# Optimization experiments

Measured on AMD Instinct MI355X. Metric: run time of the kernel, lower is better.

## Reference

```python
import jax, jax.numpy as jnp
import numpy as np

B, D = 8, 36          # batch, spatial extent of each of the 4 dims
KOUT = D - 2          # VALID conv with kernel 3 -> 34

_DN = jax.lax.ConvDimensionNumbers(lhs_spec=(0, 1, 2, 3, 4, 5),
                                   rhs_spec=(0, 1, 2, 3, 4, 5),
                                   out_spec=(0, 1, 2, 3, 4, 5))

def _conv4d(x, w):
    # x: [B, Cin, D,D,D,D], w: [Cout, Cin, 3,3,3,3] -> [B, Cout, D-2,...]
    return jax.lax.conv_general_dilated(x, w, window_strides=(1, 1, 1, 1),
                                        padding='VALID', dimension_numbers=_DN)

def setup_inputs() -> dict:
    key = jax.random.key(0)
    ks = jax.random.split(key, 8)
    fan_in = 1 * 3 ** 4  # 81 taps
    return {
        'x_real': jax.random.normal(ks[0], (B, 1, D, D, D, D), jnp.float32),
        'x_imag': jax.random.normal(ks[1], (B, 1, D, D, D, D), jnp.float32),
        'w_real': jax.random.normal(ks[2], (2, 1, 3, 3, 3, 3), jnp.float32) / np.sqrt(fan_in),
        'w_imag': jax.random.normal(ks[3], (2, 1, 3, 3, 3, 3), jnp.float32) / np.sqrt(fan_in),
        'b_real': jax.random.normal(ks[4], (2,), jnp.float32) * 0.1,
        'b_imag': jax.random.normal(ks[5], (2,), jnp.float32) * 0.1,
        'head_w': jax.random.normal(ks[6], (1, KOUT), jnp.float32) / np.sqrt(KOUT),
        'head_b': jax.random.normal(ks[7], (1,), jnp.float32) * 0.1,
    }

def reference(x_real, x_imag, w_real, w_imag, b_real, b_imag, head_w, head_b):
    bshape = (1, -1, 1, 1, 1, 1)
    # complex 4D conv: (Wr + iWi) * (xr + ixi)
    yr = _conv4d(x_real, w_real) - _conv4d(x_imag, w_imag) + b_real.reshape(bshape)
    yi = _conv4d(x_real, w_imag) + _conv4d(x_imag, w_real) + b_imag.reshape(bshape)
    # CReLU: ReLU on real and imaginary parts independently
    yr = jax.nn.relu(yr)
    yi = jax.nn.relu(yi)
    # Modulus (tiny eps keeps grad finite at 0, matching practical impls)
    m = jnp.sqrt(yr * yr + yi * yi + 1e-12)  # [B, 2, 34,34,34,34]
    # Linear(out=1) over the last spatial dim, then sigmoid
    h = jnp.einsum('bcdefw,ow->bcdefo', m, head_w) + head_b
    out = jax.nn.sigmoid(h)[:, 0]  # drop channel dim -> [B, 34, 34, 34, 1]
    return out
```

## Files before the change

kernel.cpp:

```cpp
#include <hip/hip_runtime.h>
#include <hip/hip_fp16.h>
#include <math.h>

namespace {
constexpr int DIN = 36, DOUT = 34;
constexpr int TE = 8, TF = 8;
constexpr int RE = 10, RF = 10;
constexpr int NROWS = 3*RE*RF;
constexpr int ROWW  = 38;
constexpr int NCHUNK = NROWS*9;
constexpr int BLOCKS_PER_B = 34*5*5;
constexpr int NBLOCKS = 8*BLOCKS_PER_B;
constexpr int NT = 512;
constexpr int SITER = (NCHUNK + NT - 1)/NT;
constexpr int D3 = DIN*DIN*DIN, D2 = DIN*DIN;
constexpr int WS_WPK  = 0;
constexpr int WS_SCAL = 216;
constexpr int WS_HW   = 220;
}

__device__ __forceinline__ unsigned div9u(unsigned n)   { return __umulhi(n, 0x38E38E39u) >> 1; }
__device__ __forceinline__ unsigned div100u(unsigned n) { return __umulhi(n, 0x51EB851Fu) >> 5; }
__device__ __forceinline__ unsigned div10u(unsigned n)  { return __umulhi(n, 0x66666667u) >> 2; }

__device__ __forceinline__ unsigned pack2h(float a, float b) {
    union { __half2 h; unsigned u; } x; x.h = __floats2half2_rn(a, b); return x.u;
}
__device__ __forceinline__ __half2 bch(unsigned u) {
    union { unsigned u; __half2 h; } x; x.u = u; return x.h;
}

__global__ void prep_kernel(const float* __restrict__ wr, const float* __restrict__ wi,
                            const float* __restrict__ br, const float* __restrict__ bi,
                            const float* __restrict__ hw, const float* __restrict__ hb,
                            unsigned* __restrict__ ws)
{
    const int t = threadIdx.x;
    if (t < 27) {
        uint4* p = reinterpret_cast<uint4*>(ws + WS_WPK);
        p[2*t]   = make_uint4(pack2h(wr[3*t],   -wi[3*t]),
                              pack2h(wr[3*t+1], -wi[3*t+1]),
                              pack2h(wr[3*t+2], -wi[3*t+2]), 0u);
        p[2*t+1] = make_uint4(pack2h(wi[3*t],    wr[3*t]),
                              pack2h(wi[3*t+1],  wr[3*t+1]),
                              pack2h(wi[3*t+2],  wr[3*t+2]), 0u);
    }
    if (t < DOUT) reinterpret_cast<float*>(ws)[WS_HW + t] = hw[t];
    if (t == 63) {
        float* s = reinterpret_cast<float*>(ws);
        s[WS_SCAL] = br[0]; s[WS_SCAL+1] = bi[0]; s[WS_SCAL+2] = hb[0];
    }
}

__device__ __forceinline__ void stage(const float* __restrict__ xr, const float* __restrict__ xi,
                                      unsigned* __restrict__ s_xu, int t, unsigned g0off)
{
    #pragma unroll
    for (int it = 0; it < SITER; ++it) {
        const int C = it*NT + t;
        if (C < NCHUNK) {
            const unsigned row = div9u((unsigned)C);
            const unsigned c   = (unsigned)C - row*9u;
            const unsigned rd  = div100u(row);
            const unsigned rem = row - rd*100u;
            const unsigned re  = div10u(rem);
            const unsigned rf  = rem - re*10u;
            const unsigned goff = g0off + rd*D3 + re*D2 + rf*DIN + c*4u;
            const float4 vr = *reinterpret_cast<const float4*>(xr + goff);
            const float4 vi = *reinterpret_cast<const float4*>(xi + goff);
            unsigned* dst = s_xu + row*ROWW + c*4;
            uint2 lo, hi;
            lo.x = pack2h(vr.x, vi.x); lo.y = pack2h(vr.y, vi.y);
            hi.x = pack2h(vr.z, vi.z); hi.y = pack2h(vr.w, vi.w);
            *reinterpret_cast<uint2*>(dst)     = lo;
            *reinterpret_cast<uint2*>(dst + 2) = hi;
        }
    }
}

template<int NW, int W0>
__device__ __forceinline__ float conv_group(const unsigned* __restrict__ s_xu,
                                            const uint4* __restrict__ wpk,
                                            const float* __restrict__ hws,
                                            int e, int f,
                                            float c_br, float c_bi, float hinit)
{
    constexpr int NL = (NW + 2 + 1)/2;
    __half2 accr[NW], acci[NW];
    #pragma unroll
    for (int w = 0; w < NW; ++w) {
        accr[w] = __floats2half2_rn(0.f, 0.f);
        acci[w] = __floats2half2_rn(0.f, 0.f);
    }

    const int abase = (e*RF + f)*ROWW + W0;

    #pragma unroll 1
    for (int i = 0; i < 3; ++i)
    #pragma unroll 1
    for (int j = 0; j < 3; ++j)
    {
        const unsigned* sp = s_xu + abase + (i*(RE*RF) + j*RF)*ROWW;
        const int tapb = (i*3 + j)*3;
        #pragma unroll
        for (int k = 0; k < 3; ++k)
        {
            uint2 q[NL];
            #pragma unroll
            for (int m = 0; m < NL; ++m)
                q[m] = *reinterpret_cast<const uint2*>(sp + k*ROWW + 2*m);
            const __half2* win = reinterpret_cast<const __half2*>(q);

            const uint4 wa = wpk[2*(tapb + k)];
            const uint4 wb = wpk[2*(tapb + k) + 1];
            #pragma unroll
            for (int l = 0; l < 3; ++l) {
                const __half2 WA = bch(l==0 ? wa.x : l==1 ? wa.y : wa.z);
                const __half2 WB = bch(l==0 ? wb.x : l==1 ? wb.y : wb.z);
                #pragma unroll
                for (int w = 0; w < NW; ++w) {
                    const __half2 x2 = win[w + l];
                    accr[w] = __hfma2(x2, WA, accr[w]);
                    acci[w] = __hfma2(x2, WB, acci[w]);
                }
            }
        }
    }

    float h = hinit;
    #pragma unroll
    for (int w = 0; w < NW; ++w) {
        const float yr = __low2float(accr[w]) + __high2float(accr[w]) + c_br;
        const float yi = __low2float(acci[w]) + __high2float(acci[w]) + c_bi;
        const float a = fmaxf(yr, 0.f);
        const float c = fmaxf(yi, 0.f);
        const float m = sqrtf(fmaf(a, a, fmaf(c, c, 1e-12f)));
        h = fmaf(m, hws[W0 + w], h);
    }
    return h;
}

__global__ __launch_bounds__(NT)
void lasl_kernel(const float* __restrict__ xr, const float* __restrict__ xi,
                 const unsigned* __restrict__ wsu, float* __restrict__ out)
{
    __shared__ unsigned s_xu[NROWS*ROWW];

    const int t = threadIdx.x;

    const int bid = blockIdx.x;
    const int b   = bid & 7;
    int rem = bid >> 3;
    const int d0 = rem / 25;  rem %= 25;
    const int e0 = min((rem / 5) * TE, DOUT - TE);
    const int f0 = min((rem % 5) * TF, DOUT - TF);

    const float* xrb = xr + (size_t)b * (size_t)(DIN*D3);
    const float* xib = xi + (size_t)b * (size_t)(DIN*D3);
    const unsigned g0off = (unsigned)((d0*DIN + e0)*DIN + f0)*DIN;

    stage(xrb, xib, s_xu, t, g0off);
    __syncthreads();

    const int f = t & 7;
    const int e = (t >> 3) & 7;
    const int g = t >> 6;

    const uint4* wpk = reinterpret_cast<const uint4*>(wsu + WS_WPK);
    const float* scal = reinterpret_cast<const float*>(wsu);
    const float* hws  = scal + WS_HW;
    const float c_br = scal[WS_SCAL], c_bi = scal[WS_SCAL+1];
    const float hini = (g == 0) ? scal[WS_SCAL+2] : 0.f;

    float hp;
    if      (g == 0) hp = conv_group<6, 0>(s_xu, wpk, hws, e, f, c_br, c_bi, hini);
    else if (g == 1) hp = conv_group<4, 6>(s_xu, wpk, hws, e, f, c_br, c_bi, hini);
    else if (g == 2) hp = conv_group<4,10>(s_xu, wpk, hws, e, f, c_br, c_bi, hini);
    else if (g == 3) hp = conv_group<4,14>(s_xu, wpk, hws, e, f, c_br, c_bi, hini);
    else if (g == 4) hp = conv_group<4,18>(s_xu, wpk, hws, e, f, c_br, c_bi, hini);
    else if (g == 5) hp = conv_group<4,22>(s_xu, wpk, hws, e, f, c_br, c_bi, hini);
    else if (g == 6) hp = conv_group<4,26>(s_xu, wpk, hws, e, f, c_br, c_bi, hini);
    else             hp = conv_group<4,30>(s_xu, wpk, hws, e, f, c_br, c_bi, hini);

    __syncthreads();
    float* s_red = reinterpret_cast<float*>(s_xu);
    s_red[t] = hp;
    __syncthreads();

    if (g == 0) {
        const int eg = e0 + e, fg = f0 + f;
        float htot = hp;
        #pragma unroll
        for (int gg = 1; gg < 8; ++gg) htot += s_red[t + 64*gg];
        out[(((size_t)b*DOUT + d0)*DOUT + eg)*DOUT + fg] = 1.f / (1.f + __expf(-htot));
    }
}

extern "C" void kernel_launch(void* const* d_in, const int* in_sizes, int n_in,
                              void* d_out, int out_size, void* d_ws, size_t ws_size,
                              hipStream_t stream)
{
    const float* xr = (const float*)d_in[0];
    const float* xi = (const float*)d_in[1];
    const float* wr = (const float*)d_in[2];
    const float* wi = (const float*)d_in[3];
    const float* br = (const float*)d_in[4];
    const float* bi = (const float*)d_in[5];
    const float* hw = (const float*)d_in[6];
    const float* hb = (const float*)d_in[7];
    float* out = (float*)d_out;
    unsigned* ws = (unsigned*)d_ws;

    prep_kernel<<<1, 64, 0, stream>>>(wr, wi, br, bi, hw, hb, ws);
    lasl_kernel<<<NBLOCKS, NT, 0, stream>>>(xr, xi, ws, out);
}
```

Measured before the change: 108.1 us.

## Stream d-planes through a rolling three-slot shared buffer per block

Each block now covers a segment of 8–9 output d-slices instead of one. It keeps a ring of three staged input planes in shared memory and loads only one new plane per step, so every input plane is staged once per segment rather than three times. The grid shrinks from 6800 to 800 blocks. In exchange, each block runs a serial loop with two barriers per step, has less parallelism to hide latency, and loads of the next plane do not overlap the compute of the current one. The NL window size was also reduced to match what is actually needed.

```diff
diff --git a/kernel.cpp b/kernel.cpp
--- a/kernel.cpp
+++ b/kernel.cpp
@@ -6,22 +6,21 @@
 constexpr int DIN = 36, DOUT = 34;
 constexpr int TE = 8, TF = 8;
 constexpr int RE = 10, RF = 10;
-constexpr int NROWS = 3*RE*RF;
 constexpr int ROWW  = 38;
-constexpr int NCHUNK = NROWS*9;
-constexpr int BLOCKS_PER_B = 34*5*5;
-constexpr int NBLOCKS = 8*BLOCKS_PER_B;
+constexpr int PROWS = RE*RF;
+constexpr int PDW   = PROWS*ROWW;
+constexpr int PCHUNK= PROWS*9;
+constexpr int NSEG  = 4;
+constexpr int NBLOCKS = 8*5*5*NSEG;
 constexpr int NT = 512;
-constexpr int SITER = (NCHUNK + NT - 1)/NT;
 constexpr int D3 = DIN*DIN*DIN, D2 = DIN*DIN;
 constexpr int WS_WPK  = 0;
 constexpr int WS_SCAL = 216;
 constexpr int WS_HW   = 220;
 }
 
-__device__ __forceinline__ unsigned div9u(unsigned n)   { return __umulhi(n, 0x38E38E39u) >> 1; }
-__device__ __forceinline__ unsigned div100u(unsigned n) { return __umulhi(n, 0x51EB851Fu) >> 5; }
-__device__ __forceinline__ unsigned div10u(unsigned n)  { return __umulhi(n, 0x66666667u) >> 2; }
+__device__ __forceinline__ unsigned div9u(unsigned n)  { return __umulhi(n, 0x38E38E39u) >> 1; }
+__device__ __forceinline__ unsigned div10u(unsigned n) { return __umulhi(n, 0x66666667u) >> 2; }
 
 __device__ __forceinline__ unsigned pack2h(float a, float b) {
     union { __half2 h; unsigned u; } x; x.h = __floats2half2_rn(a, b); return x.u;
@@ -52,23 +51,23 @@
     }
 }
 
-__device__ __forceinline__ void stage(const float* __restrict__ xr, const float* __restrict__ xi,
-                                      unsigned* __restrict__ s_xu, int t, unsigned g0off)
+__device__ __forceinline__ void stage_plane(const float* __restrict__ xr,
+                                            const float* __restrict__ xi,
+                                            unsigned* __restrict__ s_xu,
+                                            int t, int slot, unsigned base)
 {
     #pragma unroll
-    for (int it = 0; it < SITER; ++it) {
+    for (int it = 0; it < 2; ++it) {
         const int C = it*NT + t;
-        if (C < NCHUNK) {
+        if (C < PCHUNK) {
             const unsigned row = div9u((unsigned)C);
             const unsigned c   = (unsigned)C - row*9u;
-            const unsigned rd  = div100u(row);
-            const unsigned rem = row - rd*100u;
-            const unsigned re  = div10u(rem);
-            const unsigned rf  = rem - re*10u;
-            const unsigned goff = g0off + rd*D3 + re*D2 + rf*DIN + c*4u;
+            const unsigned re  = div10u(row);
+            const unsigned rf  = row - re*10u;
+            const unsigned goff = base + re*D2 + rf*DIN + c*4u;
             const float4 vr = *reinterpret_cast<const float4*>(xr + goff);
             const float4 vi = *reinterpret_cast<const float4*>(xi + goff);
-            unsigned* dst = s_xu + row*ROWW + c*4;
+            unsigned* dst = s_xu + slot*PDW + row*ROWW + c*4;
             uint2 lo, hi;
             lo.x = pack2h(vr.x, vi.x); lo.y = pack2h(vr.y, vi.y);
             hi.x = pack2h(vr.z, vi.z); hi.y = pack2h(vr.w, vi.w);
@@ -82,10 +81,11 @@
 __device__ __forceinline__ float conv_group(const unsigned* __restrict__ s_xu,
                                             const uint4* __restrict__ wpk,
                                             const float* __restrict__ hws,
+                                            int sl0, int sl1, int sl2,
                                             int e, int f,
                                             float c_br, float c_bi, float hinit)
 {
-    constexpr int NL = (NW + 2 + 1)/2;
+    constexpr int NL = (NW + 2)/2;
     __half2 accr[NW], acci[NW];
     #pragma unroll
     for (int w = 0; w < NW; ++w) {
@@ -93,35 +93,39 @@
         acci[w] = __floats2half2_rn(0.f, 0.f);
     }
 
-    const int abase = (e*RF + f)*ROWW + W0;
-
-    #pragma unroll 1
-    for (int i = 0; i < 3; ++i)
+    const int rbl = (e*RF + f)*ROWW + W0;
+
     #pragma unroll 1
     for (int j = 0; j < 3; ++j)
     {
-        const unsigned* sp = s_xu + abase + (i*(RE*RF) + j*RF)*ROWW;
-        const int tapb = (i*3 + j)*3;
+        const int jof = j*RF*ROWW;
         #pragma unroll
-        for (int k = 0; k < 3; ++k)
+        for (int i = 0; i < 3; ++i)
         {
-            uint2 q[NL];
+            const int sl = (i==0) ? sl0 : (i==1) ? sl1 : sl2;
+            const unsigned* sp = s_xu + sl*PDW + rbl + jof;
+            const int tapb = (i*3 + j)*3;
             #pragma unroll
-            for (int m = 0; m < NL; ++m)
-                q[m] = *reinterpret_cast<const uint2*>(sp + k*ROWW + 2*m);
-            const __half2* win = reinterpret_cast<const __half2*>(q);
-
-            const uint4 wa = wpk[2*(tapb + k)];
-            const uint4 wb = wpk[2*(tapb + k) + 1];
-            #pragma unroll
-            for (int l = 0; l < 3; ++l) {
-                const __half2 WA = bch(l==0 ? wa.x : l==1 ? wa.y : wa.z);
-                const __half2 WB = bch(l==0 ? wb.x : l==1 ? wb.y : wb.z);
+            for (int k = 0; k < 3; ++k)
+            {
+                uint2 q[NL];
                 #pragma unroll
-                for (int w = 0; w < NW; ++w) {
-                    const __half2 x2 = win[w + l];
-                    accr[w] = __hfma2(x2, WA, accr[w]);
-                    acci[w] = __hfma2(x2, WB, acci[w]);
+                for (int m = 0; m < NL; ++m)
+                    q[m] = *reinterpret_cast<const uint2*>(sp + k*ROWW + 2*m);
+                const __half2* win = reinterpret_cast<const __half2*>(q);
+
+                const uint4 wa = wpk[2*(tapb + k)];
+                const uint4 wb = wpk[2*(tapb + k) + 1];
+                #pragma unroll
+                for (int l = 0; l < 3; ++l) {
+                    const __half2 WA = bch(l==0 ? wa.x : l==1 ? wa.y : wa.z);
+                    const __half2 WB = bch(l==0 ? wb.x : l==1 ? wb.y : wb.z);
+                    #pragma unroll
+                    for (int w = 0; w < NW; ++w) {
+                        const __half2 x2 = win[w + l];
+                        accr[w] = __hfma2(x2, WA, accr[w]);
+                        acci[w] = __hfma2(x2, WB, acci[w]);
+                    }
                 }
             }
         }
@@ -144,55 +148,70 @@
 void lasl_kernel(const float* __restrict__ xr, const float* __restrict__ xi,
                  const unsigned* __restrict__ wsu, float* __restrict__ out)
 {
-    __shared__ unsigned s_xu[NROWS*ROWW];
+    __shared__ unsigned s_xu[3*PDW];
+    __shared__ float s_red[NT];
 
     const int t = threadIdx.x;
 
     const int bid = blockIdx.x;
     const int b   = bid & 7;
-    int rem = bid >> 3;
-    const int d0 = rem / 25;  rem %= 25;
-    const int e0 = min((rem / 5) * TE, DOUT - TE);
-    const int f0 = min((rem % 5) * TF, DOUT - TF);
+    const int rem = bid >> 3;
+    const int eft = rem >> 2;
+    const int seg = rem & 3;
+    const int e0 = min((eft / 5) * TE, DOUT - TE);
+    const int f0 = min((eft % 5) * TF, DOUT - TF);
+    const int d0  = (seg < 2) ? seg*9 : 18 + (seg - 2)*8;
+    const int len = (seg < 2) ? 9 : 8;
 
     const float* xrb = xr + (size_t)b * (size_t)(DIN*D3);
     const float* xib = xi + (size_t)b * (size_t)(DIN*D3);
-    const unsigned g0off = (unsigned)((d0*DIN + e0)*DIN + f0)*DIN;
-
-    stage(xrb, xib, s_xu, t, g0off);
-    __syncthreads();
+    unsigned pbase = (unsigned)(d0*D3 + e0*D2 + f0*DIN);
+
+    stage_plane(xrb, xib, s_xu, t, 0, pbase);
+    stage_plane(xrb, xib, s_xu, t, 1, pbase + D3);
+    pbase += 2*D3;
 
     const int f = t & 7;
     const int e = (t >> 3) & 7;
     const int g = t >> 6;
 
-    const uint4* wpk = reinterpret_cast<const uint4*>(wsu + WS_WPK);
+    const uint4* wpk  = reinterpret_cast<const uint4*>(wsu + WS_WPK);
     const float* scal = reinterpret_cast<const float*>(wsu);
     const float* hws  = scal + WS_HW;
     const float c_br = scal[WS_SCAL], c_bi = scal[WS_SCAL+1];
-    const float hini = (g == 0) ? scal[WS_SCAL+2] : 0.f;
-
-    float hp;
-    if      (g == 0) hp = conv_group<6, 0>(s_xu, wpk, hws, e, f, c_br, c_bi, hini);
-    else if (g == 1) hp = conv_group<4, 6>(s_xu, wpk, hws, e, f, c_br, c_bi, hini);
-    else if (g == 2) hp = conv_group<4,10>(s_xu, wpk, hws, e, f, c_br, c_bi, hini);
-    else if (g == 3) hp = conv_group<4,14>(s_xu, wpk, hws, e, f, c_br, c_bi, hini);
-    else if (g == 4) hp = conv_group<4,18>(s_xu, wpk, hws, e, f, c_br, c_bi, hini);
-    else if (g == 5) hp = conv_group<4,22>(s_xu, wpk, hws, e, f, c_br, c_bi, hini);
-    else if (g == 6) hp = conv_group<4,26>(s_xu, wpk, hws, e, f, c_br, c_bi, hini);
-    else             hp = conv_group<4,30>(s_xu, wpk, hws, e, f, c_br, c_bi, hini);
-
-    __syncthreads();
-    float* s_red = reinterpret_cast<float*>(s_xu);
-    s_red[t] = hp;
-    __syncthreads();
-
-    if (g == 0) {
-        const int eg = e0 + e, fg = f0 + f;
-        float htot = hp;
-        #pragma unroll
-        for (int gg = 1; gg < 8; ++gg) htot += s_red[t + 64*gg];
-        out[(((size_t)b*DOUT + d0)*DOUT + eg)*DOUT + fg] = 1.f / (1.f + __expf(-htot));
+    const float hb_v = scal[WS_SCAL+2];
+
+    int sl0 = 0, sl1 = 1, sl2 = 2;
+
+    for (int s = 0; s < len; ++s)
+    {
+        stage_plane(xrb, xib, s_xu, t, sl2, pbase);
+        __syncthreads();
+
+        const float hini = (g == 0) ? hb_v : 0.f;
+        float hp;
+        if      (g == 0) hp = conv_group<6, 0>(s_xu, wpk, hws, sl0, sl1, sl2, e, f, c_br, c_bi, hini);
+        else if (g == 1) hp = conv_group<4, 6>(s_xu, wpk, hws, sl0, sl1, sl2, e, f, c_br, c_bi, hini);
+        else if (g == 2) hp = conv_group<4,10>(s_xu, wpk, hws, sl0, sl1, sl2, e, f, c_br, c_bi, hini);
+        else if (g == 3) hp = conv_group<4,14>(s_xu, wpk, hws, sl0, sl1, sl2, e, f, c_br, c_bi, hini);
+        else if (g == 4) hp = conv_group<4,18>(s_xu, wpk, hws, sl0, sl1, sl2, e, f, c_br, c_bi, hini);
+        else if (g == 5) hp = conv_group<4,22>(s_xu, wpk, hws, sl0, sl1, sl2, e, f, c_br, c_bi, hini);
+        else if (g == 6) hp = conv_group<4,26>(s_xu, wpk, hws, sl0, sl1, sl2, e, f, c_br, c_bi, hini);
+        else             hp = conv_group<4,30>(s_xu, wpk, hws, sl0, sl1, sl2, e, f, c_br, c_bi, hini);
+
+        s_red[t] = hp;
+        __syncthreads();
+
+        if (g == 0) {
+            float htot = hp;
+            #pragma unroll
+            for (int gg = 1; gg < 8; ++gg) htot += s_red[t + 64*gg];
+            out[(((size_t)b*DOUT + (d0 + s))*DOUT + (e0 + e))*DOUT + (f0 + f)] =
+                1.f / (1.f + __expf(-htot));
+        }
+
+        const int tmp = sl0; sl0 = sl1; sl1 = sl2; sl2 = tmp;
+        pbase += D3;
     }
 }
 
```

New measurement: 154.3 us. 42.7% more time.

## Retile output as 4x4x4 cubes over d,e,f to cut halo staging

Applied to the files above, without the earlier changes.

Each block now computes a 4x4x4 cube of (d,e,f) output positions instead of a 1x8x8 slab. This shrinks the staged input halo from 300 rows to 216 rows per 64 outputs and reduces the block count, lowering global loads and LDS footprint. The reduction buffer gets its own shared array. Edge tiles are clamped, so some outputs are computed and written twice with identical values.

```diff
diff --git a/kernel.cpp b/kernel.cpp
--- a/kernel.cpp
+++ b/kernel.cpp
@@ -4,12 +4,12 @@
 
 namespace {
 constexpr int DIN = 36, DOUT = 34;
-constexpr int TE = 8, TF = 8;
-constexpr int RE = 10, RF = 10;
-constexpr int NROWS = 3*RE*RF;
+constexpr int RT = 6;
+constexpr int NROWS = RT*RT*RT;
 constexpr int ROWW  = 38;
 constexpr int NCHUNK = NROWS*9;
-constexpr int BLOCKS_PER_B = 34*5*5;
+constexpr int NTILE = 9;
+constexpr int BLOCKS_PER_B = NTILE*NTILE*NTILE;
 constexpr int NBLOCKS = 8*BLOCKS_PER_B;
 constexpr int NT = 512;
 constexpr int SITER = (NCHUNK + NT - 1)/NT;
@@ -19,9 +19,8 @@
 constexpr int WS_HW   = 220;
 }
 
-__device__ __forceinline__ unsigned div9u(unsigned n)   { return __umulhi(n, 0x38E38E39u) >> 1; }
-__device__ __forceinline__ unsigned div100u(unsigned n) { return __umulhi(n, 0x51EB851Fu) >> 5; }
-__device__ __forceinline__ unsigned div10u(unsigned n)  { return __umulhi(n, 0x66666667u) >> 2; }
+__device__ __forceinline__ unsigned div9u(unsigned n) { return __umulhi(n, 0x38E38E39u) >> 1; }
+__device__ __forceinline__ unsigned div6u(unsigned n) { return __umulhi(n, 0xAAAAAAABu) >> 2; }
 
 __device__ __forceinline__ unsigned pack2h(float a, float b) {
     union { __half2 h; unsigned u; } x; x.h = __floats2half2_rn(a, b); return x.u;
@@ -61,10 +60,10 @@
         if (C < NCHUNK) {
             const unsigned row = div9u((unsigned)C);
             const unsigned c   = (unsigned)C - row*9u;
-            const unsigned rd  = div100u(row);
-            const unsigned rem = row - rd*100u;
-            const unsigned re  = div10u(rem);
-            const unsigned rf  = rem - re*10u;
+            const unsigned rd  = div9u(row) >> 2;
+            const unsigned rem = row - rd*36u;
+            const unsigned re  = div6u(rem);
+            const unsigned rf  = rem - re*6u;
             const unsigned goff = g0off + rd*D3 + re*D2 + rf*DIN + c*4u;
             const float4 vr = *reinterpret_cast<const float4*>(xr + goff);
             const float4 vi = *reinterpret_cast<const float4*>(xi + goff);
@@ -82,10 +81,10 @@
 __device__ __forceinline__ float conv_group(const unsigned* __restrict__ s_xu,
                                             const uint4* __restrict__ wpk,
                                             const float* __restrict__ hws,
-                                            int e, int f,
+                                            int d, int e, int f,
                                             float c_br, float c_bi, float hinit)
 {
-    constexpr int NL = (NW + 2 + 1)/2;
+    constexpr int NL = (NW + 2)/2;
     __half2 accr[NW], acci[NW];
     #pragma unroll
     for (int w = 0; w < NW; ++w) {
@@ -93,14 +92,12 @@
         acci[w] = __floats2half2_rn(0.f, 0.f);
     }
 
-    const int abase = (e*RF + f)*ROWW + W0;
-
     #pragma unroll 1
     for (int i = 0; i < 3; ++i)
     #pragma unroll 1
     for (int j = 0; j < 3; ++j)
     {
-        const unsigned* sp = s_xu + abase + (i*(RE*RF) + j*RF)*ROWW;
+        const unsigned* sp = s_xu + (((d+i)*RT + (e+j))*RT + f)*ROWW + W0;
         const int tapb = (i*3 + j)*3;
         #pragma unroll
         for (int k = 0; k < 3; ++k)
@@ -145,15 +142,19 @@
                  const unsigned* __restrict__ wsu, float* __restrict__ out)
 {
     __shared__ unsigned s_xu[NROWS*ROWW];
+    __shared__ float s_red[NT];
 
     const int t = threadIdx.x;
 
     const int bid = blockIdx.x;
     const int b   = bid & 7;
     int rem = bid >> 3;
-    const int d0 = rem / 25;  rem %= 25;
-    const int e0 = min((rem / 5) * TE, DOUT - TE);
-    const int f0 = min((rem % 5) * TF, DOUT - TF);
+    const int dt = rem / 81;  rem -= dt*81;
+    const int et = rem / 9;
+    const int ft = rem - (rem/9)*9;
+    const int d0 = min(4*dt, 30);
+    const int e0 = min(4*et, 30);
+    const int f0 = min(4*ft, 30);
 
     const float* xrb = xr + (size_t)b * (size_t)(DIN*D3);
     const float* xib = xi + (size_t)b * (size_t)(DIN*D3);
@@ -162,37 +163,37 @@
     stage(xrb, xib, s_xu, t, g0off);
     __syncthreads();
 
-    const int f = t & 7;
-    const int e = (t >> 3) & 7;
+    const int f = t & 3;
+    const int e = (t >> 2) & 3;
+    const int d = (t >> 4) & 3;
     const int g = t >> 6;
 
-    const uint4* wpk = reinterpret_cast<const uint4*>(wsu + WS_WPK);
+    const uint4* wpk  = reinterpret_cast<const uint4*>(wsu + WS_WPK);
     const float* scal = reinterpret_cast<const float*>(wsu);
     const float* hws  = scal + WS_HW;
     const float c_br = scal[WS_SCAL], c_bi = scal[WS_SCAL+1];
     const float hini = (g == 0) ? scal[WS_SCAL+2] : 0.f;
 
     float hp;
-    if      (g == 0) hp = conv_group<6, 0>(s_xu, wpk, hws, e, f, c_br, c_bi, hini);
-    else if (g == 1) hp = conv_group<4, 6>(s_xu, wpk, hws, e, f, c_br, c_bi, hini);
-    else if (g == 2) hp = conv_group<4,10>(s_xu, wpk, hws, e, f, c_br, c_bi, hini);
-    else if (g == 3) hp = conv_group<4,14>(s_xu, wpk, hws, e, f, c_br, c_bi, hini);
-    else if (g == 4) hp = conv_group<4,18>(s_xu, wpk, hws, e, f, c_br, c_bi, hini);
-    else if (g == 5) hp = conv_group<4,22>(s_xu, wpk, hws, e, f, c_br, c_bi, hini);
-    else if (g == 6) hp = conv_group<4,26>(s_xu, wpk, hws, e, f, c_br, c_bi, hini);
-    else             hp = conv_group<4,30>(s_xu, wpk, hws, e, f, c_br, c_bi, hini);
+    if      (g == 0) hp = conv_group<6, 0>(s_xu, wpk, hws, d, e, f, c_br, c_bi, hini);
+    else if (g == 1) hp = conv_group<4, 6>(s_xu, wpk, hws, d, e, f, c_br, c_bi, hini);
+    else if (g == 2) hp = conv_group<4,10>(s_xu, wpk, hws, d, e, f, c_br, c_bi, hini);
+    else if (g == 3) hp = conv_group<4,14>(s_xu, wpk, hws, d, e, f, c_br, c_bi, hini);
+    else if (g == 4) hp = conv_group<4,18>(s_xu, wpk, hws, d, e, f, c_br, c_bi, hini);
+    else if (g == 5) hp = conv_group<4,22>(s_xu, wpk, hws, d, e, f, c_br, c_bi, hini);
+    else if (g == 6) hp = conv_group<4,26>(s_xu, wpk, hws, d, e, f, c_br, c_bi, hini);
+    else             hp = conv_group<4,30>(s_xu, wpk, hws, d, e, f, c_br, c_bi, hini);
 
     __syncthreads();
-    float* s_red = reinterpret_cast<float*>(s_xu);
     s_red[t] = hp;
     __syncthreads();
 
     if (g == 0) {
-        const int eg = e0 + e, fg = f0 + f;
         float htot = hp;
         #pragma unroll
         for (int gg = 1; gg < 8; ++gg) htot += s_red[t + 64*gg];
-        out[(((size_t)b*DOUT + d0)*DOUT + eg)*DOUT + fg] = 1.f / (1.f + __expf(-htot));
+        out[(((size_t)b*DOUT + (d0 + d))*DOUT + (e0 + e))*DOUT + (f0 + f)] =
+            1.f / (1.f + __expf(-htot));
     }
 }
 
```

Result: faster. 90.74 us, median of 2 (-16.1%).
